# Performance work log

Hardware: AMD Instinct MI355X
Metric: run time of the kernel (lower is better)

Reference implementation:

```python
import jax, jax.numpy as jnp
import numpy as np

N, NFEAT, NHID, NCLASS = 8192, 512, 256, 16
ALPHA = 0.01          # LeakyReLU negative slope
NEG = -9.0e15         # mask fill value from the original code
ADJ_DENSITY = 0.01    # ~82 neighbors per node


def setup_inputs() -> dict:
    key = jax.random.key(0)
    ks = jax.random.split(key, 9)
    x = jax.random.normal(ks[0], (N, NFEAT), jnp.float32)
    # sparse binary adjacency with self-loops, stored dense as in the torch code
    adj = (jax.random.uniform(ks[1], (N, N)) < ADJ_DENSITY).astype(jnp.int32)
    adj = adj.at[jnp.arange(N), jnp.arange(N)].set(1)
    s = 0.05
    W1 = jax.random.normal(ks[2], (NFEAT, NHID), jnp.float32) * s   # gc1.weight
    b1 = jax.random.normal(ks[3], (NHID,), jnp.float32) * s         # gc1.bias
    Wa = jax.random.normal(ks[4], (NHID, NHID), jnp.float32) * s    # out_att.W (nhid*nheads -> nhid)
    a_vec = jax.random.normal(ks[5], (2 * NHID, 1), jnp.float32) * s  # out_att.a
    W3 = jax.random.normal(ks[6], (NHID, NCLASS), jnp.float32) * s  # gc3.weight
    b3 = jax.random.normal(ks[7], (NCLASS,), jnp.float32) * s       # gc3.bias
    return {"x": x, "adj": adj, "W1": W1, "b1": b1, "Wa": Wa,
            "a_vec": a_vec, "W3": W3, "b3": b3}


def reference(x, adj, W1, b1, Wa, a_vec, W3, b3):
    adjf = adj.astype(x.dtype)
    # gc1: spmm(adj, x @ W1) + b1, then ReLU  (eval mode -> dropout is identity)
    h1 = jax.nn.relu(adjf @ (x @ W1) + b1)        # [N, NHID]
    feat = h1
    # out_att (GraphAttentionLayer, concat=False)
    Wh = h1 @ Wa                                   # [N, NHID]
    f1 = Wh @ a_vec[:NHID]                         # [N, 1]
    f2 = Wh @ a_vec[NHID:]                         # [N, 1]
    e = jax.nn.leaky_relu(f1 + f2.T, ALPHA)        # dense [N, N] scores
    e = jnp.where(adj > 0, e, jnp.asarray(NEG, x.dtype))
    attention = jax.nn.softmax(e, axis=1)          # row-wise masked softmax
    h_prime = attention @ Wh                       # [N, NHID]
    a_out = jax.nn.elu(h_prime)                    # x = F.elu(a)
    # gc3
    out = adjf @ (a_out @ W3) + b3                 # [N, NCLASS]
    return (jax.nn.sigmoid(out), attention, jnp.concatenate([feat, out], axis=1))
```

## Files before the change

kernel.cpp:

```cpp
#include <hip/hip_runtime.h>
#include <hip/hip_bf16.h>

#define NN    8192
#define NFEAT 512
#define NHID  256
#define NCLASS 16
#define ELLW  256

typedef __hip_bfloat16 bf16;
typedef unsigned short u16;
typedef __bf16 bf16x8 __attribute__((ext_vector_type(8)));
typedef float  f32x4  __attribute__((ext_vector_type(4)));
typedef int    i32x4  __attribute__((ext_vector_type(4)));

__global__ __launch_bounds__(256) void probe_dtype2(const u16* __restrict__ a, int na,
                                                    const u16* __restrict__ b, int nb,
                                                    int* __restrict__ cnt) {
  int c = 0;
  for (int i = blockIdx.x * 256 + threadIdx.x; i < na; i += gridDim.x * 256)
    if (((a[i] >> 7) & 0xFF) == 0xFF) c++;
  for (int i = blockIdx.x * 256 + threadIdx.x; i < nb; i += gridDim.x * 256)
    if (((b[i] >> 7) & 0xFF) == 0xFF) c++;
  if (c) atomicAdd(cnt, c);
}

__global__ __launch_bounds__(256) void convert_bf(const void* __restrict__ src,
                                                  bf16* __restrict__ dst, int n,
                                                  const int* __restrict__ flagcnt) {
  bool isf32 = (*flagcnt > 16);
  int i = blockIdx.x * 256 + threadIdx.x;
  if (i < n) {
    if (isf32) dst[i] = __float2bfloat16(((const float*)src)[i]);
    else       dst[i] = ((const bf16*)src)[i];
  }
}

__global__ __launch_bounds__(256) void convert_rest(const void* __restrict__ W1r,
                                                    const void* __restrict__ War,
                                                    const void* __restrict__ b1r,
                                                    const void* __restrict__ avr,
                                                    const void* __restrict__ W3r,
                                                    const void* __restrict__ b3r,
                                                    bf16* __restrict__ W1t,
                                                    bf16* __restrict__ Wat,
                                                    float* __restrict__ b1f,
                                                    float* __restrict__ avecf,
                                                    float* __restrict__ W3f,
                                                    float* __restrict__ b3f,
                                                    const int* __restrict__ flagcnt) {
  bool isf32 = (*flagcnt > 16);
  auto rd = [&](const void* p, int i) -> float {
    return isf32 ? ((const float*)p)[i] : __bfloat162float(((const bf16*)p)[i]);
  };
  const int n1 = NFEAT * NHID;
  const int n2 = n1 + NHID * NHID;
  const int n3 = n2 + NHID;
  const int n4 = n3 + 2 * NHID;
  const int n5 = n4 + NHID * NCLASS;
  const int n6 = n5 + NCLASS;
  for (int i = blockIdx.x * 256 + threadIdx.x; i < n6; i += gridDim.x * 256) {
    if (i < n1)      { int k = i / NHID, n = i % NHID; W1t[(size_t)n * NFEAT + k] = __float2bfloat16(rd(W1r, i)); }
    else if (i < n2) { int j = i - n1; int k = j / NHID, n = j % NHID; Wat[(size_t)n * NHID + k] = __float2bfloat16(rd(War, j)); }
    else if (i < n3) b1f[i - n2] = rd(b1r, i - n2);
    else if (i < n4) avecf[i - n3] = rd(avr, i - n3);
    else if (i < n5) W3f[i - n4] = rd(W3r, i - n4);
    else             b3f[i - n5] = rd(b3r, i - n5);
  }
}

__global__ __launch_bounds__(256) void build_ell(const int* __restrict__ adj,
                                                 int* __restrict__ ell_cnt,
                                                 u16* __restrict__ ell_col) {
  __shared__ int cnt;
  int row = blockIdx.x;
  if (threadIdx.x == 0) cnt = 0;
  __syncthreads();
  const i32x4* arow = (const i32x4*)(adj + (size_t)row * NN);
  u16* crow = ell_col + (size_t)row * ELLW;
  int lane = threadIdx.x & 63;
  unsigned long long lt = ((unsigned long long)1 << lane) - 1;
  for (int j4 = threadIdx.x; j4 < NN / 4; j4 += 256) {
    i32x4 v = __builtin_nontemporal_load(&arow[j4]);
    unsigned long long m0 = __ballot(v.x != 0);
    unsigned long long m1 = __ballot(v.y != 0);
    unsigned long long m2 = __ballot(v.z != 0);
    unsigned long long m3 = __ballot(v.w != 0);
    int c0 = __popcll(m0), c1 = __popcll(m1), c2 = __popcll(m2), c3 = __popcll(m3);
    int total = c0 + c1 + c2 + c3;
    int base = 0;
    if (lane == 0 && total) base = atomicAdd(&cnt, total);
    base = __shfl(base, 0, 64);
    int col = j4 * 4;
    if (v.x) { int p = base + __popcll(m0 & lt);                 if (p < ELLW) crow[p] = (u16)col;       }
    if (v.y) { int p = base + c0 + __popcll(m1 & lt);            if (p < ELLW) crow[p] = (u16)(col + 1); }
    if (v.z) { int p = base + c0 + c1 + __popcll(m2 & lt);       if (p < ELLW) crow[p] = (u16)(col + 2); }
    if (v.w) { int p = base + c0 + c1 + c2 + __popcll(m3 & lt);  if (p < ELLW) crow[p] = (u16)(col + 3); }
  }
  __syncthreads();
  if (threadIdx.x == 0) ell_cnt[row] = cnt < ELLW ? cnt : ELLW;
}

#define TM 64
#define TN 64
#define LDSP 72

__global__ __launch_bounds__(256) void gemm_bt(const bf16* __restrict__ A, int lda,
                                               const bf16* __restrict__ Bt, int ldb,
                                               bf16* __restrict__ C, int ldc, int K) {
  __shared__ __align__(16) bf16 sA[TM * LDSP];
  __shared__ __align__(16) bf16 sB[TN * LDSP];
  int bm = blockIdx.x, bn = blockIdx.y;
  int t = threadIdx.x;
  int wave = t >> 6, lane = t & 63;
  int quad = lane >> 4, l16 = lane & 15;
  f32x4 acc[4] = {};

  int srow = t >> 2;
  int sk   = (t & 3) * 16;
  const size_t abase = (size_t)(bm * TM + srow) * lda + sk;
  const size_t bbase = (size_t)(bn * TN + srow) * ldb + sk;

  uint4 pa0 = *(const uint4*)&A[abase];
  uint4 pa1 = *(const uint4*)&A[abase + 8];
  uint4 pb0 = *(const uint4*)&Bt[bbase];
  uint4 pb1 = *(const uint4*)&Bt[bbase + 8];

  for (int kt = 0; kt < K; kt += 64) {
    *(uint4*)&sA[srow * LDSP + sk]     = pa0;
    *(uint4*)&sA[srow * LDSP + sk + 8] = pa1;
    *(uint4*)&sB[srow * LDSP + sk]     = pb0;
    *(uint4*)&sB[srow * LDSP + sk + 8] = pb1;
    __syncthreads();
    if (kt + 64 < K) {
      pa0 = *(const uint4*)&A[abase + kt + 64];
      pa1 = *(const uint4*)&A[abase + kt + 72];
      pb0 = *(const uint4*)&Bt[bbase + kt + 64];
      pb1 = *(const uint4*)&Bt[bbase + kt + 72];
    }
    bf16x8 af0 = *(const bf16x8*)&sA[(wave * 16 + l16) * LDSP + quad * 8];
    bf16x8 af1 = *(const bf16x8*)&sA[(wave * 16 + l16) * LDSP + 32 + quad * 8];
#pragma unroll
    for (int c = 0; c < 4; ++c) {
      bf16x8 bf0 = *(const bf16x8*)&sB[(c * 16 + l16) * LDSP + quad * 8];
      bf16x8 bf1 = *(const bf16x8*)&sB[(c * 16 + l16) * LDSP + 32 + quad * 8];
      acc[c] = __builtin_amdgcn_mfma_f32_16x16x32_bf16(af0, bf0, acc[c], 0, 0, 0);
      acc[c] = __builtin_amdgcn_mfma_f32_16x16x32_bf16(af1, bf1, acc[c], 0, 0, 0);
    }
    __syncthreads();
  }
  int row0 = bm * TM + wave * 16 + quad * 4;
  int col0 = bn * TN;
#pragma unroll
  for (int c = 0; c < 4; ++c) {
#pragma unroll
    for (int r = 0; r < 4; ++r) {
      C[(size_t)(row0 + r) * ldc + col0 + c * 16 + l16] = __float2bfloat16(acc[c][r]);
    }
  }
}

__global__ __launch_bounds__(256) void spmm_h1(const bf16* __restrict__ XW,
                                               const int* __restrict__ ell_cnt,
                                               const u16* __restrict__ ell_col,
                                               const float* __restrict__ b1,
                                               float* __restrict__ out2,
                                               bf16* __restrict__ h1b) {
  __shared__ int sc0[ELLW], sc1[ELLW];
  int r0 = blockIdx.x * 2, r1 = r0 + 1;
  int t = threadIdx.x;
  int nn0 = ell_cnt[r0], nn1 = ell_cnt[r1];
  const u16* c0 = ell_col + (size_t)r0 * ELLW;
  const u16* c1 = ell_col + (size_t)r1 * ELLW;
  for (int k = t; k < nn0; k += 256) sc0[k] = c0[k];
  for (int k = t; k < nn1; k += 256) sc1[k] = c1[k];
  __syncthreads();
  float a0 = 0.f, a1 = 0.f;
#pragma unroll 4
  for (int k = 0; k < nn0; ++k) a0 += __bfloat162float(XW[(size_t)sc0[k] * NHID + t]);
#pragma unroll 4
  for (int k = 0; k < nn1; ++k) a1 += __bfloat162float(XW[(size_t)sc1[k] * NHID + t]);
  float bb = b1[t];
  a0 = fmaxf(a0 + bb, 0.f);
  a1 = fmaxf(a1 + bb, 0.f);
  out2[(size_t)r0 * (NHID + NCLASS) + t] = a0;
  out2[(size_t)r1 * (NHID + NCLASS) + t] = a1;
  h1b[(size_t)r0 * NHID + t] = __float2bfloat16(a0);
  h1b[(size_t)r1 * NHID + t] = __float2bfloat16(a1);
}

__global__ __launch_bounds__(256) void f12_kernel(const bf16* __restrict__ Wh,
                                                  const float* __restrict__ avec,
                                                  float* __restrict__ f12) {
  int wave = threadIdx.x >> 6, lane = threadIdx.x & 63;
  int row = blockIdx.x * 4 + wave;
  const bf16* wr = Wh + (size_t)row * NHID;
  float s1 = 0.f, s2 = 0.f;
  for (int k = lane; k < NHID; k += 64) {
    float w = __bfloat162float(wr[k]);
    s1 += w * avec[k];
    s2 += w * avec[NHID + k];
  }
  for (int o = 32; o > 0; o >>= 1) {
    s1 += __shfl_down(s1, o, 64);
    s2 += __shfl_down(s2, o, 64);
  }
  if (lane == 0) { f12[row] = s1; f12[NN + row] = s2; }
}

__global__ __launch_bounds__(256) void attn_fused(const bf16* __restrict__ Wh,
                                                  const int* __restrict__ ell_cnt,
                                                  const u16* __restrict__ ell_col,
                                                  const float* __restrict__ f12,
                                                  float* __restrict__ att,
                                                  bf16* __restrict__ aout) {
  __shared__ float p[ELLW];
  __shared__ int scols[ELLW];
  __shared__ float red[8];
  int row = blockIdx.x, t = threadIdx.x;
  int nn = ell_cnt[row];
  const u16* cr = ell_col + (size_t)row * ELLW;
  float f1i = f12[row];
  const float* f2 = f12 + NN;

  f32x4* dst = (f32x4*)(att + (size_t)row * NN);
  f32x4 z = {0.f, 0.f, 0.f, 0.f};
#pragma unroll
  for (int k = t; k < NN / 4; k += 256) __builtin_nontemporal_store(z, &dst[k]);

  for (int k = t; k < nn; k += 256) scols[k] = cr[k];
  __syncthreads();

  float lmax = -1e30f;
  for (int k = t; k < nn; k += 256) {
    float e = f1i + f2[scols[k]];
    e = (e > 0.f) ? e : 0.01f * e;
    p[k] = e;
    lmax = fmaxf(lmax, e);
  }
  for (int o = 32; o > 0; o >>= 1) lmax = fmaxf(lmax, __shfl_down(lmax, o, 64));
  if ((t & 63) == 0) red[t >> 6] = lmax;
  __syncthreads();
  float gmax = fmaxf(fmaxf(red[0], red[1]), fmaxf(red[2], red[3]));

  float lsum = 0.f;
  for (int k = t; k < nn; k += 256) {
    float ex = __expf(p[k] - gmax);
    p[k] = ex;
    lsum += ex;
  }
  for (int o = 32; o > 0; o >>= 1) lsum += __shfl_down(lsum, o, 64);
  __syncthreads();
  if ((t & 63) == 0) red[4 + (t >> 6)] = lsum;
  __syncthreads();
  float inv = 1.f / fmaxf(red[4] + red[5] + red[6] + red[7], 1e-30f);

  for (int k = t; k < nn; k += 256)
    att[(size_t)row * NN + scols[k]] = p[k] * inv;

  float acc = 0.f;
#pragma unroll 8
  for (int k = 0; k < nn; ++k)
    acc += p[k] * __bfloat162float(Wh[(size_t)scols[k] * NHID + t]);
  acc *= inv;
  float e = (acc > 0.f) ? acc : (__expf(acc) - 1.f);
  aout[(size_t)row * NHID + t] = __float2bfloat16(e);
}

__global__ __launch_bounds__(256) void attn_sparse(const bf16* __restrict__ Wh,
                                                   const int* __restrict__ ell_cnt,
                                                   const u16* __restrict__ ell_col,
                                                   const float* __restrict__ f12,
                                                   bf16* __restrict__ aout) {
  __shared__ float p[ELLW];
  __shared__ int scols[ELLW];
  __shared__ float red[8];
  int row = blockIdx.x, t = threadIdx.x;
  int nn = ell_cnt[row];
  const u16* cr = ell_col + (size_t)row * ELLW;
  float f1i = f12[row];
  const float* f2 = f12 + NN;
  for (int k = t; k < nn; k += 256) scols[k] = cr[k];
  __syncthreads();
  float lmax = -1e30f;
  for (int k = t; k < nn; k += 256) {
    float e = f1i + f2[scols[k]];
    e = (e > 0.f) ? e : 0.01f * e;
    p[k] = e;
    lmax = fmaxf(lmax, e);
  }
  for (int o = 32; o > 0; o >>= 1) lmax = fmaxf(lmax, __shfl_down(lmax, o, 64));
  if ((t & 63) == 0) red[t >> 6] = lmax;
  __syncthreads();
  float gmax = fmaxf(fmaxf(red[0], red[1]), fmaxf(red[2], red[3]));
  float lsum = 0.f;
  for (int k = t; k < nn; k += 256) {
    float ex = __expf(p[k] - gmax);
    p[k] = ex;
    lsum += ex;
  }
  for (int o = 32; o > 0; o >>= 1) lsum += __shfl_down(lsum, o, 64);
  __syncthreads();
  if ((t & 63) == 0) red[4 + (t >> 6)] = lsum;
  __syncthreads();
  float inv = 1.f / fmaxf(red[4] + red[5] + red[6] + red[7], 1e-30f);
  float acc = 0.f;
  for (int k = 0; k < nn; ++k)
    acc += p[k] * __bfloat162float(Wh[(size_t)scols[k] * NHID + t]);
  acc *= inv;
  float e = (acc > 0.f) ? acc : (__expf(acc) - 1.f);
  aout[(size_t)row * NHID + t] = __float2bfloat16(e);
}

__global__ __launch_bounds__(256) void attn_dense(const int* __restrict__ adj,
                                                  const float* __restrict__ f12,
                                                  float* __restrict__ att) {
  __shared__ __align__(16) float rowbuf[NN];
  __shared__ float se[ELLW];
  __shared__ int sj[ELLW];
  __shared__ float red[8];
  __shared__ int cnt;
  int row = blockIdx.x, t = threadIdx.x;
  if (t == 0) cnt = 0;
  f32x4* rb4 = (f32x4*)rowbuf;
  f32x4 z = {0.f, 0.f, 0.f, 0.f};
  for (int k = t; k < NN / 4; k += 256) rb4[k] = z;
  float f1i = f12[row];
  const float* f2 = f12 + NN;
  __syncthreads();
  const int4* arow = (const int4*)(adj + (size_t)row * NN);
  for (int j4 = t; j4 < NN / 4; j4 += 256) {
    int4 v = arow[j4];
    int base = j4 * 4;
    if (v.x) { int p = atomicAdd(&cnt, 1); if (p < ELLW) { sj[p] = base;     se[p] = f1i + f2[base];     } }
    if (v.y) { int p = atomicAdd(&cnt, 1); if (p < ELLW) { sj[p] = base + 1; se[p] = f1i + f2[base + 1]; } }
    if (v.z) { int p = atomicAdd(&cnt, 1); if (p < ELLW) { sj[p] = base + 2; se[p] = f1i + f2[base + 2]; } }
    if (v.w) { int p = atomicAdd(&cnt, 1); if (p < ELLW) { sj[p] = base + 3; se[p] = f1i + f2[base + 3]; } }
  }
  __syncthreads();
  int nn = cnt < ELLW ? cnt : ELLW;
  float lmax = -1e30f;
  for (int k = t; k < nn; k += 256) {
    float e = se[k];
    e = (e > 0.f) ? e : 0.01f * e;
    se[k] = e;
    lmax = fmaxf(lmax, e);
  }
  for (int o = 32; o > 0; o >>= 1) lmax = fmaxf(lmax, __shfl_down(lmax, o, 64));
  if ((t & 63) == 0) red[t >> 6] = lmax;
  __syncthreads();
  float gmax = fmaxf(fmaxf(red[0], red[1]), fmaxf(red[2], red[3]));
  float lsum = 0.f;
  for (int k = t; k < nn; k += 256) {
    float ex = __expf(se[k] - gmax);
    se[k] = ex;
    lsum += ex;
  }
  for (int o = 32; o > 0; o >>= 1) lsum += __shfl_down(lsum, o, 64);
  __syncthreads();
  if ((t & 63) == 0) red[4 + (t >> 6)] = lsum;
  __syncthreads();
  float inv = 1.f / fmaxf(red[4] + red[5] + red[6] + red[7], 1e-30f);
  for (int k = t; k < nn; k += 256) rowbuf[sj[k]] = se[k] * inv;
  __syncthreads();
  const f32x4* src = (const f32x4*)rowbuf;
  f32x4* dst = (f32x4*)(att + (size_t)row * NN);
  for (int k = t; k < NN / 4; k += 256) dst[k] = src[k];
}

__global__ __launch_bounds__(256) void gemm3(const bf16* __restrict__ aout,
                                             const float* __restrict__ W3,
                                             float* __restrict__ A3) {
  __shared__ float sW[NHID * NCLASS];
  __shared__ bf16 sa[16 * NHID];
  int t = threadIdx.x;
  for (int k = t; k < NHID * NCLASS; k += 256) sW[k] = W3[k];
  int r0 = blockIdx.x * 16;
  for (int k = t; k < 16 * NHID; k += 256) sa[k] = aout[(size_t)r0 * NHID + k];
  __syncthreads();
  int r = t >> 4, c = t & 15;
  float acc = 0.f;
#pragma unroll 8
  for (int k = 0; k < NHID; ++k)
    acc += __bfloat162float(sa[r * NHID + k]) * sW[k * NCLASS + c];
  A3[(size_t)(r0 + r) * NCLASS + c] = acc;
}

__global__ __launch_bounds__(256) void spmm_out2(const float* __restrict__ A3,
                                                 const int* __restrict__ ell_cnt,
                                                 const u16* __restrict__ ell_col,
                                                 const float* __restrict__ b3,
                                                 float* __restrict__ out2,
                                                 float* __restrict__ out0,
                                                 int write_sig) {
  int g = blockIdx.x * 256 + threadIdx.x;
  int row = g >> 4, c = g & 15;
  int nn = ell_cnt[row];
  const u16* cr = ell_col + (size_t)row * ELLW;
  float acc = b3[c];
#pragma unroll 8
  for (int k = 0; k < nn; ++k)
    acc += A3[(size_t)cr[k] * NCLASS + c];
  out2[(size_t)row * (NHID + NCLASS) + NHID + c] = acc;
  if (write_sig) out0[g] = 1.f / (1.f + __expf(-acc));
}

__global__ __launch_bounds__(256) void copy_f32(const float* __restrict__ src,
                                                float* __restrict__ dst, int n) {
  int i = blockIdx.x * 256 + threadIdx.x;
  if (i < n) dst[i] = src[i];
}

__global__ __launch_bounds__(256) void sigmoid_from_out2(const float* __restrict__ out2,
                                                         float* __restrict__ out0) {
  int g = blockIdx.x * 256 + threadIdx.x;
  int row = g >> 4, c = g & 15;
  float v = out2[(size_t)row * (NHID + NCLASS) + NHID + c];
  out0[g] = 1.f / (1.f + __expf(-v));
}

extern "C" void kernel_launch(void* const* d_in, const int* in_sizes, int n_in,
                              void* d_out, int out_size, void* d_ws, size_t ws_size,
                              hipStream_t stream) {
  const void* x_raw    = d_in[0];
  const int*  adj      = (const int*)d_in[1];
  const void* W1_raw   = d_in[2];
  const void* b1_raw   = d_in[3];
  const void* Wa_raw   = d_in[4];
  const void* avec_raw = d_in[5];
  const void* W3_raw   = d_in[6];
  const void* b3_raw   = d_in[7];

  float* out0 = (float*)d_out;
  float* out1 = out0 + (size_t)NN * NCLASS;
  float* out2 = out1 + (size_t)NN * NN;

  const size_t NEED = 36u << 20;
  bool useWS = (d_ws != nullptr) && (ws_size >= NEED);

  char* a = useWS ? (char*)d_ws : (char*)out1;
  size_t o = 0;
  auto carve = [&](size_t bytes) { char* p = a + o; o += (bytes + 4095) & ~(size_t)4095; return p; };
  int*   flag    = (int*)  carve(4096);
  int*   ell_cnt = (int*)  carve((size_t)NN * 4);
  u16*   ell_col = (u16*)  carve((size_t)NN * ELLW * 2);
  bf16*  xc      = (bf16*) carve((size_t)NN * NFEAT * 2);
  bf16*  W1t     = (bf16*) carve((size_t)NHID * NFEAT * 2);
  bf16*  Wat     = (bf16*) carve((size_t)NHID * NHID * 2);
  float* avecf   = (float*)carve((size_t)2 * NHID * 4);
  float* b1f     = (float*)carve((size_t)NHID * 4);
  float* b3f     = (float*)carve((size_t)NCLASS * 4);
  float* W3f     = (float*)carve((size_t)NHID * NCLASS * 4);
  bf16*  XW      = (bf16*) carve((size_t)NN * NHID * 2);
  bf16*  h1b     = (bf16*) carve((size_t)NN * NHID * 2);
  bf16*  Wh      = (bf16*) carve((size_t)NN * NHID * 2);
  float* f12a    = (float*)carve((size_t)2 * NN * 4);
  bf16*  aout    = (bf16*) carve((size_t)NN * NHID * 2);
  float* A3ws    = (float*)carve((size_t)NN * NCLASS * 4);

  float* A3 = useWS ? A3ws : out0;
  float* f12stash = out0;

  (void)hipMemsetAsync(flag, 0, 4, stream);
  probe_dtype2<<<128, 256, 0, stream>>>((const u16*)x_raw, NN * NFEAT,
                                        (const u16*)W1_raw, NFEAT * NHID, flag);
  convert_bf<<<(NN * NFEAT + 255) / 256, 256, 0, stream>>>(x_raw, xc, NN * NFEAT, flag);
  convert_rest<<<256, 256, 0, stream>>>(W1_raw, Wa_raw, b1_raw, avec_raw, W3_raw, b3_raw,
                                        W1t, Wat, b1f, avecf, W3f, b3f, flag);

  build_ell<<<NN, 256, 0, stream>>>(adj, ell_cnt, ell_col);
  gemm_bt<<<dim3(NN / TM, NHID / TN), 256, 0, stream>>>(xc, NFEAT, W1t, NFEAT, XW, NHID, NFEAT);
  spmm_h1<<<NN / 2, 256, 0, stream>>>(XW, ell_cnt, ell_col, b1f, out2, h1b);
  gemm_bt<<<dim3(NN / TM, NHID / TN), 256, 0, stream>>>(h1b, NHID, Wat, NHID, Wh, NHID, NHID);
  f12_kernel<<<NN / 4, 256, 0, stream>>>(Wh, avecf, f12a);

  if (useWS) {
    attn_fused<<<NN, 256, 0, stream>>>(Wh, ell_cnt, ell_col, f12a, out1, aout);
    gemm3<<<NN / 16, 256, 0, stream>>>(aout, W3f, A3);
    spmm_out2<<<NN * NCLASS / 256, 256, 0, stream>>>(A3, ell_cnt, ell_col, b3f, out2, out0, 1);
  } else {
    attn_sparse<<<NN, 256, 0, stream>>>(Wh, ell_cnt, ell_col, f12a, aout);
    gemm3<<<NN / 16, 256, 0, stream>>>(aout, W3f, A3);
    spmm_out2<<<NN * NCLASS / 256, 256, 0, stream>>>(A3, ell_cnt, ell_col, b3f, out2, out0, 0);
    copy_f32<<<(2 * NN + 255) / 256, 256, 0, stream>>>(f12a, f12stash, 2 * NN);
    attn_dense<<<NN, 256, 0, stream>>>(adj, f12stash, out1);
    sigmoid_from_out2<<<NN * NCLASS / 256, 256, 0, stream>>>(out2, out0);
  }
}
```

Baseline: 642.6 us.

## Stage attention rows in LDS and fuse gc3 GEMM with sparse aggregation

The attention kernel now builds each 8192-wide row in shared memory (zeros plus scattered softmax values) and writes it out with one coalesced nontemporal store pass. This replaces the zero-store pass followed by scattered global writes. Separately, gc3 is reordered as (adj·a_out)·W3 in a single per-row kernel, replacing gemm3 plus spmm_out2. The 32KB of LDS per block may lower occupancy, and the new gc3 gathers 256-wide bf16 rows per neighbor instead of 16-wide fp32 rows, which adds gather traffic.

```diff
diff --git a/kernel.cpp b/kernel.cpp
--- a/kernel.cpp
+++ b/kernel.cpp
@@ -213,6 +213,7 @@
                                                   const float* __restrict__ f12,
                                                   float* __restrict__ att,
                                                   bf16* __restrict__ aout) {
+  __shared__ __align__(16) float rowbuf[NN];
   __shared__ float p[ELLW];
   __shared__ int scols[ELLW];
   __shared__ float red[8];
@@ -222,11 +223,10 @@
   float f1i = f12[row];
   const float* f2 = f12 + NN;
 
-  f32x4* dst = (f32x4*)(att + (size_t)row * NN);
+  f32x4* rb4 = (f32x4*)rowbuf;
   f32x4 z = {0.f, 0.f, 0.f, 0.f};
 #pragma unroll
-  for (int k = t; k < NN / 4; k += 256) __builtin_nontemporal_store(z, &dst[k]);
-
+  for (int k = t; k < NN / 4; k += 256) rb4[k] = z;
   for (int k = t; k < nn; k += 256) scols[k] = cr[k];
   __syncthreads();
 
@@ -254,8 +254,11 @@
   __syncthreads();
   float inv = 1.f / fmaxf(red[4] + red[5] + red[6] + red[7], 1e-30f);
 
-  for (int k = t; k < nn; k += 256)
-    att[(size_t)row * NN + scols[k]] = p[k] * inv;
+  for (int k = t; k < nn; k += 256) rowbuf[scols[k]] = p[k] * inv;
+  __syncthreads();
+  f32x4* dst = (f32x4*)(att + (size_t)row * NN);
+#pragma unroll
+  for (int k = t; k < NN / 4; k += 256) __builtin_nontemporal_store(rb4[k], &dst[k]);
 
   float acc = 0.f;
 #pragma unroll 8
@@ -264,6 +267,44 @@
   acc *= inv;
   float e = (acc > 0.f) ? acc : (__expf(acc) - 1.f);
   aout[(size_t)row * NHID + t] = __float2bfloat16(e);
+}
+
+__global__ __launch_bounds__(256) void spmm_gc3(const bf16* __restrict__ aout,
+                                                const int* __restrict__ ell_cnt,
+                                                const u16* __restrict__ ell_col,
+                                                const float* __restrict__ W3,
+                                                const float* __restrict__ b3,
+                                                float* __restrict__ out2,
+                                                float* __restrict__ out0) {
+  __shared__ float sW[NHID * NCLASS];
+  __shared__ float s[NHID];
+  __shared__ int scols[ELLW];
+  int row = blockIdx.x, t = threadIdx.x;
+  int nn = ell_cnt[row];
+  const u16* cr = ell_col + (size_t)row * ELLW;
+  for (int k = t; k < NHID * NCLASS; k += 256) sW[k] = W3[k];
+  for (int k = t; k < nn; k += 256) scols[k] = cr[k];
+  __syncthreads();
+  float acc = 0.f;
+#pragma unroll 8
+  for (int k = 0; k < nn; ++k)
+    acc += __bfloat162float(aout[(size_t)scols[k] * NHID + t]);
+  s[t] = acc;
+  __syncthreads();
+  int c = t >> 4, j = t & 15;
+  float part = 0.f;
+#pragma unroll
+  for (int k = j; k < NHID; k += 16)
+    part += s[k] * sW[k * NCLASS + c];
+  part += __shfl_down(part, 8, 64);
+  part += __shfl_down(part, 4, 64);
+  part += __shfl_down(part, 2, 64);
+  part += __shfl_down(part, 1, 64);
+  if (j == 0) {
+    float v = part + b3[c];
+    out2[(size_t)row * (NHID + NCLASS) + NHID + c] = v;
+    out0[(size_t)row * NCLASS + c] = 1.f / (1.f + __expf(-v));
+  }
 }
 
 __global__ __launch_bounds__(256) void attn_sparse(const bf16* __restrict__ Wh,
@@ -475,8 +516,7 @@
 
   if (useWS) {
     attn_fused<<<NN, 256, 0, stream>>>(Wh, ell_cnt, ell_col, f12a, out1, aout);
-    gemm3<<<NN / 16, 256, 0, stream>>>(aout, W3f, A3);
-    spmm_out2<<<NN * NCLASS / 256, 256, 0, stream>>>(A3, ell_cnt, ell_col, b3f, out2, out0, 1);
+    spmm_gc3<<<NN, 256, 0, stream>>>(aout, ell_cnt, ell_col, W3f, b3f, out2, out0);
   } else {
     attn_sparse<<<NN, 256, 0, stream>>>(Wh, ell_cnt, ell_col, f12a, aout);
     gemm3<<<NN / 16, 256, 0, stream>>>(aout, W3f, A3);
```

New measurement: 654.9 us. No clear change (+1.9%).
